# Performance work log

Measured on AMD Instinct MI355X. Metric: run time of the kernel, lower is better.

The kernel has to match this reference:

```python
import jax, jax.numpy as jnp
import numpy as np

B, NPG = 128, 128          # graphs, nodes per graph
N = B * NPG                # total nodes
K = 16                     # kNN neighbors within cutoff
D = 256                    # embedding_depth
H, DH = 4, 32              # heads = num_layers, head dim = (D//2)//H
L = 4                      # num graph convolutions
NR = 50                    # num_radial
CUTOFF = 2.0
OUT = 3 + 100              # 3 + max_ntypes


def setup_inputs() -> dict:
    rng = np.random.default_rng(0)
    pos = rng.standard_normal((N, 3)).astype(np.float32)
    nbrs = np.zeros((N, K), np.int32)
    mask = np.zeros((N, K), np.float32)
    for g in range(B):  # per-graph kNN with radial cutoff (setup only, numpy)
        p = pos[g * NPG:(g + 1) * NPG]
        d2 = ((p[:, None, :] - p[None, :, :]) ** 2).sum(-1)
        np.fill_diagonal(d2, np.inf)
        idx = np.argsort(d2, axis=1)[:, :K]
        dk = np.sqrt(np.take_along_axis(d2, idx, 1))
        nbrs[g * NPG:(g + 1) * NPG] = idx + g * NPG
        mask[g * NPG:(g + 1) * NPG] = (dk <= CUTOFF).astype(np.float32)
    batch_idx = np.repeat(np.arange(B, dtype=np.int32), NPG)

    key = jax.random.key(0)
    ks = jax.random.split(key, 12)
    s = 0.02
    return {
        'encoding': jax.random.normal(ks[0], (B, D), jnp.float32),
        'pos': jnp.asarray(pos),
        'batch_idx': jnp.asarray(batch_idx),
        'neighbors': jnp.asarray(nbrs),
        'nbr_mask': jnp.asarray(mask),
        'W_in': jax.random.normal(ks[1], (D + 3, D), jnp.float32) * s,
        'b_in': jnp.zeros((D,), jnp.float32),
        'Wq': jax.random.normal(ks[2], (L, D, H * DH), jnp.float32) * s,
        'Wk': jax.random.normal(ks[3], (L, D, H * DH), jnp.float32) * s,
        'Wv': jax.random.normal(ks[4], (L, D, H * DH), jnp.float32) * s,
        'We': jax.random.normal(ks[5], (L, NR, H * DH), jnp.float32) * s,
        'Wo': jax.random.normal(ks[6], (L, H * DH, D), jnp.float32) * s,
        'bo': jnp.zeros((L, D), jnp.float32),
        'Wfc': jax.random.normal(ks[7], (L, D, D), jnp.float32) * s,
        'bfc': jnp.zeros((L, D), jnp.float32),
        'ln_g': jnp.ones((L, D), jnp.float32),
        'ln_b': jnp.zeros((L, D), jnp.float32),
        'W_out': jax.random.normal(ks[8], (D, OUT), jnp.float32) * s,
        'b_out': jnp.zeros((OUT,), jnp.float32),
    }


def reference(encoding, pos, batch_idx, neighbors, nbr_mask,
              W_in, b_in, Wq, Wk, Wv, We, Wo, bo, Wfc, bfc,
              ln_g, ln_b, W_out, b_out):
    # x = encoding.repeat_interleave(graph_sizes); x[:, 0] = 1
    x = encoding[batch_idx]                      # [N, D]
    x = x.at[:, 0].set(1.0)
    h = jnp.concatenate([x, pos], axis=-1) @ W_in + b_in   # concat pos, embed

    # gaussian radial basis of neighbor distances
    dvec = pos[neighbors] - pos[:, None, :]      # [N, K, 3]
    d = jnp.sqrt((dvec ** 2).sum(-1) + 1e-12)    # [N, K]
    centers = jnp.linspace(0.0, CUTOFF, NR)
    width = centers[1] - centers[0]
    rbf = jnp.exp(-0.5 * ((d[..., None] - centers) / width) ** 2)  # [N, K, NR]

    scale = 1.0 / jnp.sqrt(jnp.float32(DH))
    m = nbr_mask[..., None]                      # [N, K, 1]
    for l in range(L):                           # TransformerConv layers
        q = (h @ Wq[l]).reshape(N, H, DH)
        k = (h @ Wk[l]).reshape(N, H, DH)
        v = (h @ Wv[l]).reshape(N, H, DH)
        e = (rbf @ We[l]).reshape(N, K, H, DH)   # edge embedding
        kj = k[neighbors] + e                    # [N, K, H, DH]
        vj = v[neighbors] + e
        logits = jnp.einsum('nhd,nkhd->nkh', q, kj) * scale
        logits = jnp.where(m > 0, logits, -1e9)
        a = jax.nn.softmax(logits, axis=1) * m   # masked attention over K
        msg = jnp.einsum('nkh,nkhd->nhd', a, vj).reshape(N, H * DH)
        h = h + msg @ Wo[l] + bo[l]              # residual update
        mu = h.mean(-1, keepdims=True)
        var = h.var(-1, keepdims=True)
        h = ln_g[l] * (h - mu) / jnp.sqrt(var + 1e-5) + ln_b[l]
        h = jax.nn.gelu(h @ Wfc[l] + bfc[l])     # nodewise fc (1 layer)

    return h @ W_out + b_out                     # [N, 3 + max_ntypes]
```

## Files before the change

### kernel.cpp

```cpp
#include <hip/hip_runtime.h>
#include <hip/hip_bf16.h>
#include <math.h>

#define N_PTS 16384
#define NLAYER 4

typedef __attribute__((ext_vector_type(8))) short bfrag;
typedef __attribute__((ext_vector_type(4))) float f32x4;
typedef unsigned short ushort_t;
typedef unsigned int uint_t;

__device__ __forceinline__ ushort_t f2b(float f) {
  __hip_bfloat16 h = __float2bfloat16(f);
  return *reinterpret_cast<const ushort_t*>(&h);
}
__device__ __forceinline__ float b2f(ushort_t u) {
  union { uint_t i; float f; } c; c.i = ((uint_t)u) << 16; return c.f;
}
__device__ __forceinline__ float blo(uint_t u) {
  union { uint_t i; float f; } c; c.i = u << 16; return c.f;
}
__device__ __forceinline__ float bhi(uint_t u) {
  union { uint_t i; float f; } c; c.i = u & 0xffff0000u; return c.f;
}

__global__ __launch_bounds__(256) void base_kernel(
    const float* __restrict__ enc, const float* __restrict__ W_in,
    const float* __restrict__ b_in, float* __restrict__ base)
{
  int b = blockIdx.x, j = threadIdx.x;
  __shared__ float se[256];
  se[j] = enc[b * 256 + j];
  __syncthreads();
  float acc = b_in[j] + W_in[j];
  for (int i = 1; i < 256; ++i) acc += se[i] * W_in[i * 256 + j];
  base[b * 256 + j] = acc;
}

__global__ __launch_bounds__(256) void embed_kernel(
    const float* __restrict__ base, const int* __restrict__ batch_idx,
    const float* __restrict__ pos, const float* __restrict__ W_in,
    ushort_t* __restrict__ h_bf)
{
  int n = blockIdx.x, j = threadIdx.x;
  int b = batch_idx[n];
  float px = pos[n * 3 + 0], py = pos[n * 3 + 1], pz = pos[n * 3 + 2];
  float v = base[b * 256 + j]
      + px * W_in[256 * 256 + j] + py * W_in[257 * 256 + j] + pz * W_in[258 * 256 + j];
  h_bf[(size_t)n * 256 + j] = f2b(v);
}

__global__ __launch_bounds__(256) void prep_qkv(
    const float* __restrict__ Wq, const float* __restrict__ Wk,
    const float* __restrict__ Wv, const float* __restrict__ We,
    ushort_t* __restrict__ out)
{
  int idx = blockIdx.x * 256 + threadIdx.x;
  int l = idx / (640 * 256);
  int rem = idx - l * (640 * 256);
  int j = rem >> 8, k = rem & 255;
  float v = 0.f;
  if (j < 128) v = Wq[((size_t)l * 256 + k) * 128 + j];
  else if (j < 328) {
    int p = j - 128, hq = p / 50, r = p - hq * 50;
    const float* wq = &Wq[((size_t)l * 256 + k) * 128 + hq * 32];
    const float* we = &We[((size_t)l * 50 + r) * 128 + hq * 32];
#pragma unroll
    for (int d = 0; d < 32; ++d) v += wq[d] * we[d];
  } else if (j < 456) v = Wk[((size_t)l * 256 + k) * 128 + (j - 328)];
  else if (j < 584) v = Wv[((size_t)l * 256 + k) * 128 + (j - 456)];
  out[idx] = f2b(v);
}

__global__ __launch_bounds__(256) void prep_bcat(
    const float* __restrict__ We, const float* __restrict__ Wo, ushort_t* __restrict__ out)
{
  int idx = blockIdx.x * 256 + threadIdx.x;
  int l = idx / (256 * 384);
  int rem = idx - l * (256 * 384);
  int j = rem / 384, k2 = rem - j * 384;
  float v = 0.f;
  if (k2 < 128) v = Wo[((size_t)l * 128 + k2) * 256 + j];
  else if (k2 < 328) {
    int p = k2 - 128, hq = p / 50, r = p - hq * 50;
    const float* we = &We[((size_t)l * 50 + r) * 128 + hq * 32];
    const float* wo = &Wo[((size_t)l * 128 + hq * 32) * 256 + j];
#pragma unroll
    for (int d = 0; d < 32; ++d) v += we[d] * wo[(size_t)d * 256];
  }
  out[idx] = f2b(v);
}

__global__ __launch_bounds__(256) void prep_wfc(
    const float* __restrict__ Wfc, ushort_t* __restrict__ out)
{
  int idx = blockIdx.x * 256 + threadIdx.x;
  int l = idx >> 16, rem = idx & 65535;
  int j = rem >> 8, k = rem & 255;
  out[idx] = f2b(Wfc[((size_t)l * 256 + k) * 256 + j]);
}

__global__ __launch_bounds__(256) void prep_wout(
    const float* __restrict__ W_out, ushort_t* __restrict__ out)
{
  int idx = blockIdx.x * 256 + threadIdx.x;
  int j = idx >> 8, k = idx & 255;
  out[idx] = (j < 103) ? f2b(W_out[(size_t)k * 103 + j]) : (ushort_t)0;
}

template<int MODE>
__global__ __launch_bounds__(512, 4) void fused_layer(
    const ushort_t* __restrict__ A0,
    const ushort_t* __restrict__ BcT,
    const float* __restrict__ bo,
    ushort_t* __restrict__ hb,
    const float* __restrict__ lg, const float* __restrict__ lb,
    const ushort_t* __restrict__ WfT,
    const float* __restrict__ bfc,
    const ushort_t* __restrict__ W3T,
    const float* __restrict__ b3,
    ushort_t* __restrict__ qext_b, ushort_t* __restrict__ kvb,
    float* __restrict__ outF)
{
  __shared__ __align__(16) ushort_t sA[32 * 384];
  __shared__ __align__(16) ushort_t sH[32 * 256];
  __shared__ float pS[8][32], pSS[8][32];

  const int tid = threadIdx.x;
  const int bid = blockIdx.x;
  const int lane = tid & 63, w = tid >> 6;
  const int l15 = lane & 15, l4 = lane >> 4;
  const int m0 = ((bid & 7) + 8 * ((bid >> 3) & 15)) * 128 + (bid >> 7) * 32;
  const int r7 = l15 & 7;

  f32x4 acc[2][2];

  if constexpr (MODE != 2) {
    for (int i = tid; i < 32 * 48; i += 512) {
      int r = i / 48, c8 = i - r * 48;
      uint4 v = (uint4){0, 0, 0, 0};
      if (c8 < 44) v = *(const uint4*)(A0 + (size_t)(m0 + r) * 352 + c8 * 8);
      *(uint4*)(&sA[r * 384 + ((c8 ^ (r & 7)) << 3)]) = v;
    }
    __syncthreads();

#pragma unroll
    for (int m = 0; m < 2; ++m) {
      acc[m][0] = (f32x4){0.f, 0.f, 0.f, 0.f};
      acc[m][1] = (f32x4){0.f, 0.f, 0.f, 0.f};
    }
    {
      const ushort_t* bB0 = BcT + (size_t)(w * 32 + l15) * 384 + l4 * 8;
      const ushort_t* bB1 = bB0 + 16 * 384;
#pragma unroll
      for (int k0 = 0; k0 < 352; k0 += 32) {
        const int ch = (k0 >> 3) + l4;
        bfrag a0 = *(const bfrag*)(sA + (0 * 16 + l15) * 384 + ((ch ^ r7) << 3));
        bfrag a1 = *(const bfrag*)(sA + (1 * 16 + l15) * 384 + ((ch ^ r7) << 3));
        bfrag b0 = *(const bfrag*)(bB0 + k0);
        bfrag b1 = *(const bfrag*)(bB1 + k0);
        acc[0][0] = __builtin_amdgcn_mfma_f32_16x16x32_bf16(a0, b0, acc[0][0], 0, 0, 0);
        acc[0][1] = __builtin_amdgcn_mfma_f32_16x16x32_bf16(a0, b1, acc[0][1], 0, 0, 0);
        acc[1][0] = __builtin_amdgcn_mfma_f32_16x16x32_bf16(a1, b0, acc[1][0], 0, 0, 0);
        acc[1][1] = __builtin_amdgcn_mfma_f32_16x16x32_bf16(a1, b1, acc[1][1], 0, 0, 0);
      }
    }

    const int c0 = w * 32 + l15, c1 = c0 + 16;
    {
      const float bo0 = bo[c0], bo1 = bo[c1];
#pragma unroll
      for (int m = 0; m < 2; ++m)
#pragma unroll
        for (int i = 0; i < 4; ++i) {
          const int rl = m * 16 + l4 * 4 + i;
          const size_t r = (size_t)(m0 + rl);
          float x0 = acc[m][0][i] + bo0 + b2f(hb[r * 256 + c0]);
          float x1 = acc[m][1][i] + bo1 + b2f(hb[r * 256 + c1]);
          acc[m][0][i] = x0; acc[m][1][i] = x1;
          float s = x0 + x1, ss = x0 * x0 + x1 * x1;
          s += __shfl_xor(s, 1, 64); ss += __shfl_xor(ss, 1, 64);
          s += __shfl_xor(s, 2, 64); ss += __shfl_xor(ss, 2, 64);
          s += __shfl_xor(s, 4, 64); ss += __shfl_xor(ss, 4, 64);
          s += __shfl_xor(s, 8, 64); ss += __shfl_xor(ss, 8, 64);
          if (l15 == 0) { pS[w][rl] = s; pSS[w][rl] = ss; }
        }
    }
    __syncthreads();
    {
      const float g0 = lg[c0], g1 = lg[c1];
      const float b0 = lb[c0], b1 = lb[c1];
      const int ch0 = c0 >> 3, ch1 = c1 >> 3;
#pragma unroll
      for (int m = 0; m < 2; ++m)
#pragma unroll
        for (int i = 0; i < 4; ++i) {
          const int rl = m * 16 + l4 * 4 + i;
          float s = 0.f, ss = 0.f;
#pragma unroll
          for (int w2 = 0; w2 < 8; ++w2) { s += pS[w2][rl]; ss += pSS[w2][rl]; }
          float mu = s * (1.f / 256.f);
          float var = ss * (1.f / 256.f) - mu * mu;
          float inv = 1.0f / sqrtf(var + 1e-5f);
          sH[rl * 256 + (((ch0 ^ (rl & 7)) << 3) | (c0 & 7))] =
              f2b(g0 * (acc[m][0][i] - mu) * inv + b0);
          sH[rl * 256 + (((ch1 ^ (rl & 7)) << 3) | (c1 & 7))] =
              f2b(g1 * (acc[m][1][i] - mu) * inv + b1);
        }
    }
    __syncthreads();

#pragma unroll
    for (int m = 0; m < 2; ++m) {
      acc[m][0] = (f32x4){0.f, 0.f, 0.f, 0.f};
      acc[m][1] = (f32x4){0.f, 0.f, 0.f, 0.f};
    }
    {
      const ushort_t* bB0 = WfT + (size_t)(w * 32 + l15) * 256 + l4 * 8;
      const ushort_t* bB1 = bB0 + 16 * 256;
#pragma unroll
      for (int k0 = 0; k0 < 256; k0 += 32) {
        const int ch = (k0 >> 3) + l4;
        bfrag a0 = *(const bfrag*)(sH + (0 * 16 + l15) * 256 + ((ch ^ r7) << 3));
        bfrag a1 = *(const bfrag*)(sH + (1 * 16 + l15) * 256 + ((ch ^ r7) << 3));
        bfrag b0 = *(const bfrag*)(bB0 + k0);
        bfrag b1 = *(const bfrag*)(bB1 + k0);
        acc[0][0] = __builtin_amdgcn_mfma_f32_16x16x32_bf16(a0, b0, acc[0][0], 0, 0, 0);
        acc[0][1] = __builtin_amdgcn_mfma_f32_16x16x32_bf16(a0, b1, acc[0][1], 0, 0, 0);
        acc[1][0] = __builtin_amdgcn_mfma_f32_16x16x32_bf16(a1, b0, acc[1][0], 0, 0, 0);
        acc[1][1] = __builtin_amdgcn_mfma_f32_16x16x32_bf16(a1, b1, acc[1][1], 0, 0, 0);
      }
    }

    {
      const float bf0 = bfc[c0], bf1 = bfc[c1];
      const int ch0 = c0 >> 3, ch1 = c1 >> 3;
#pragma unroll
      for (int m = 0; m < 2; ++m)
#pragma unroll
        for (int i = 0; i < 4; ++i) {
          const int rl = m * 16 + l4 * 4 + i;
          const size_t r = (size_t)(m0 + rl);
          float x0 = acc[m][0][i] + bf0;
          float x1 = acc[m][1][i] + bf1;
          float t0 = tanhf(0.7978845608028654f * (x0 + 0.044715f * x0 * x0 * x0));
          float t1 = tanhf(0.7978845608028654f * (x1 + 0.044715f * x1 * x1 * x1));
          float gl0 = 0.5f * x0 * (1.f + t0);
          float gl1 = 0.5f * x1 * (1.f + t1);
          ushort_t u0 = f2b(gl0), u1 = f2b(gl1);
          hb[r * 256 + c0] = u0;
          hb[r * 256 + c1] = u1;
          sA[rl * 256 + (((ch0 ^ (rl & 7)) << 3) | (c0 & 7))] = u0;
          sA[rl * 256 + (((ch1 ^ (rl & 7)) << 3) | (c1 & 7))] = u1;
        }
    }
    __syncthreads();
  } else {
    for (int i = tid; i < 32 * 32; i += 512) {
      int r = i >> 5, c8 = i & 31;
      *(uint4*)(&sA[r * 256 + ((c8 ^ (r & 7)) << 3)]) =
          *(const uint4*)(A0 + (size_t)(m0 + r) * 256 + c8 * 8);
    }
    __syncthreads();
  }

  const int NB = (MODE == 1) ? 1 : 5;
  for (int nb = 0; nb < NB; ++nb) {
    f32x4 a3[2];
    a3[0] = (f32x4){0.f, 0.f, 0.f, 0.f};
    a3[1] = (f32x4){0.f, 0.f, 0.f, 0.f};
    const ushort_t* bB = W3T + (size_t)(nb * 128 + w * 16 + l15) * 256 + l4 * 8;
#pragma unroll
    for (int k0 = 0; k0 < 256; k0 += 32) {
      const int ch = (k0 >> 3) + l4;
      bfrag a0 = *(const bfrag*)(sA + (0 * 16 + l15) * 256 + ((ch ^ r7) << 3));
      bfrag a1 = *(const bfrag*)(sA + (1 * 16 + l15) * 256 + ((ch ^ r7) << 3));
      bfrag b0 = *(const bfrag*)(bB + k0);
      a3[0] = __builtin_amdgcn_mfma_f32_16x16x32_bf16(a0, b0, a3[0], 0, 0, 0);
      a3[1] = __builtin_amdgcn_mfma_f32_16x16x32_bf16(a1, b0, a3[1], 0, 0, 0);
    }
    const int c = nb * 128 + w * 16 + l15;
#pragma unroll
    for (int m = 0; m < 2; ++m)
#pragma unroll
      for (int i = 0; i < 4; ++i) {
        const size_t r = (size_t)(m0 + m * 16 + l4 * 4 + i);
        float v = a3[m][i];
        if constexpr (MODE == 1) {
          if (c < 103) outF[r * 103 + c] = v + b3[c];
        } else {
          if (c < 328) qext_b[r * 352 + c] = f2b(v);
          else if (c < 584) kvb[r * 256 + (c - 328)] = f2b(v);
        }
      }
  }
}

__global__ __launch_bounds__(256) void attn_kernel(
    const ushort_t* __restrict__ qext, const ushort_t* __restrict__ kvb,
    const float* __restrict__ pos, const int* __restrict__ nbrs,
    const float* __restrict__ mask, ushort_t* __restrict__ Amsg)
{
  __shared__ __align__(16) ushort_t sQ[4][128];
  __shared__ __align__(16) float    sQE[4][4][52];
  __shared__ __align__(16) ushort_t sRbf[4][16][52];
  __shared__ float sA[4][64];
  __shared__ float sD[4][16];
  __shared__ float sMk[4][16];
  __shared__ int   sNb[4][16];

  const int tid = threadIdx.x;
  const int bid = blockIdx.x;
  const int lane = tid & 63, w = tid >> 6;
  const int g = (bid & 7) + 8 * ((bid >> 3) & 15);
  const int q4 = bid >> 7;
  const int kk = lane >> 2, hh = lane & 3;

  for (int it = 0; it < 4; ++it) {
    const int n = g * 128 + q4 * 16 + w * 4 + it;
    if (lane < 16) {
      int nb = nbrs[n * 16 + lane];
      sNb[w][lane] = nb;
      sMk[w][lane] = mask[n * 16 + lane];
      float dx = pos[nb * 3 + 0] - pos[n * 3 + 0];
      float dy = pos[nb * 3 + 1] - pos[n * 3 + 1];
      float dz = pos[nb * 3 + 2] - pos[n * 3 + 2];
      sD[w][lane] = sqrtf(dx * dx + dy * dy + dz * dz + 1e-12f);
      sRbf[w][lane][50] = 0; sRbf[w][lane][51] = 0;
      *(uint4*)(&sQ[w][lane * 8]) = *(const uint4*)(qext + (size_t)n * 352 + lane * 8);
    }
    if (lane < 50) {
      uint2 u = *(const uint2*)(qext + (size_t)n * 352 + 128 + lane * 4);
      int p = lane * 4;
#pragma unroll
      for (int e = 0; e < 4; ++e) {
        ushort_t bb = ((const ushort_t*)&u)[e];
        int pp = p + e, h2 = pp / 50, r = pp - h2 * 50;
        sQE[w][h2][r] = b2f(bb);
      }
    }
    if (lane < 8) sQE[w][lane >> 1][50 + (lane & 1)] = 0.f;
    {
      int kk2 = lane & 15;
      float dk = sD[w][kk2];
      int r0 = lane >> 4;
#pragma unroll
      for (int j = 0; j < 13; ++j) {
        int r = r0 + j * 4;
        if (r < 50) {
          float t = (dk - (2.f / 49.f) * (float)r) * 24.5f;
          sRbf[w][kk2][r] = f2b(__expf(-0.5f * t * t));
        }
      }
    }
    const int nb = sNb[w][kk];
    const ushort_t* krow = kvb + (size_t)nb * 256 + hh * 32;
    float qk = 0.f;
#pragma unroll
    for (int c8 = 0; c8 < 4; ++c8) {
      uint4 kv4 = *(const uint4*)(krow + c8 * 8);
      const uint_t* q4p = (const uint_t*)(&sQ[w][hh * 32 + c8 * 8]);
      uint_t qa = q4p[0], qb = q4p[1], qc = q4p[2], qd = q4p[3];
      qk += blo(qa) * blo(kv4.x) + bhi(qa) * bhi(kv4.x)
          + blo(qb) * blo(kv4.y) + bhi(qb) * bhi(kv4.y)
          + blo(qc) * blo(kv4.z) + bhi(qc) * bhi(kv4.z)
          + blo(qd) * blo(kv4.w) + bhi(qd) * bhi(kv4.w);
    }
    float qe = 0.f;
#pragma unroll
    for (int c = 0; c < 13; ++c) {
      float4 qv = *(const float4*)(&sQE[w][hh][c * 4]);
      uint2 rv = *(const uint2*)(&sRbf[w][kk][c * 4]);
      qe += qv.x * blo(rv.x) + qv.y * bhi(rv.x)
          + qv.z * blo(rv.y) + qv.w * bhi(rv.y);
    }
    float lg = 0.17677669529663687f * (qk + qe);
    lg = (sMk[w][kk] > 0.f) ? lg : -1e9f;

    float mx = lg;
#pragma unroll
    for (int off = 4; off < 64; off <<= 1) mx = fmaxf(mx, __shfl_xor(mx, off, 64));
    float ex = __expf(lg - mx);
    float sm = ex;
#pragma unroll
    for (int off = 4; off < 64; off <<= 1) sm += __shfl_xor(sm, off, 64);
    sA[w][kk * 4 + hh] = ex / sm * sMk[w][kk];

    if (lane < 50) {
      float r0 = 0.f, r1 = 0.f, r2 = 0.f, r3 = 0.f;
#pragma unroll
      for (int k2 = 0; k2 < 16; ++k2) {
        float rb = b2f(sRbf[w][k2][lane]);
        r0 += sA[w][k2 * 4 + 0] * rb;
        r1 += sA[w][k2 * 4 + 1] * rb;
        r2 += sA[w][k2 * 4 + 2] * rb;
        r3 += sA[w][k2 * 4 + 3] * rb;
      }
      Amsg[(size_t)n * 352 + 128 + 0 * 50 + lane] = f2b(r0);
      Amsg[(size_t)n * 352 + 128 + 1 * 50 + lane] = f2b(r1);
      Amsg[(size_t)n * 352 + 128 + 2 * 50 + lane] = f2b(r2);
      Amsg[(size_t)n * 352 + 128 + 3 * 50 + lane] = f2b(r3);
    }
    {
      const int h2 = lane >> 4;
      float m0v = 0.f, m1v = 0.f;
#pragma unroll
      for (int k2 = 0; k2 < 16; ++k2) {
        int nb2 = sNb[w][k2];
        uint_t vv = *(const uint_t*)(kvb + (size_t)nb2 * 256 + 128 + lane * 2);
        float a = sA[w][k2 * 4 + h2];
        m0v += a * blo(vv);
        m1v += a * bhi(vv);
      }
      uint_t o = (uint_t)f2b(m0v) | ((uint_t)f2b(m1v) << 16);
      *(uint_t*)(&Amsg[(size_t)n * 352 + lane * 2]) = o;
    }
    if (lane < 24) Amsg[(size_t)n * 352 + 328 + lane] = 0;
  }
}

extern "C" void kernel_launch(void* const* d_in, const int* in_sizes, int n_in,
                              void* d_out, int out_size, void* d_ws, size_t ws_size,
                              hipStream_t stream) {
  const float* enc    = (const float*)d_in[0];
  const float* pos    = (const float*)d_in[1];
  const int*   bidx   = (const int*)  d_in[2];
  const int*   nbrs   = (const int*)  d_in[3];
  const float* mask   = (const float*)d_in[4];
  const float* W_in   = (const float*)d_in[5];
  const float* b_in   = (const float*)d_in[6];
  const float* Wq     = (const float*)d_in[7];
  const float* Wk     = (const float*)d_in[8];
  const float* Wv     = (const float*)d_in[9];
  const float* We     = (const float*)d_in[10];
  const float* Wo     = (const float*)d_in[11];
  const float* bo     = (const float*)d_in[12];
  const float* Wfc    = (const float*)d_in[13];
  const float* bfc    = (const float*)d_in[14];
  const float* ln_g   = (const float*)d_in[15];
  const float* ln_b   = (const float*)d_in[16];
  const float* W_out  = (const float*)d_in[17];
  const float* b_out  = (const float*)d_in[18];
  float* out = (float*)d_out;

  const int N = N_PTS;
  ushort_t* ws = (ushort_t*)d_ws;
  ushort_t* hb     = ws;
  ushort_t* qext_b = hb + (size_t)N * 256;
  ushort_t* kvb    = qext_b + (size_t)N * 352;
  ushort_t* Amsg   = kvb + (size_t)N * 256;
  float*    base   = (float*)(Amsg + (size_t)N * 352);
  ushort_t* WqkvT  = (ushort_t*)(base + 128 * 256);
  ushort_t* BcT    = WqkvT + 4 * 640 * 256;
  ushort_t* WfT    = BcT  + 4 * 256 * 384;
  ushort_t* WoT    = WfT  + 4 * 256 * 256;

  base_kernel<<<128, 256, 0, stream>>>(enc, W_in, b_in, base);
  embed_kernel<<<N, 256, 0, stream>>>(base, bidx, pos, W_in, hb);
  prep_qkv<<<(4 * 640 * 256) / 256, 256, 0, stream>>>(Wq, Wk, Wv, We, WqkvT);
  prep_bcat<<<(4 * 256 * 384) / 256, 256, 0, stream>>>(We, Wo, BcT);
  prep_wfc<<<(4 * 256 * 256) / 256, 256, 0, stream>>>(Wfc, WfT);
  prep_wout<<<(128 * 256) / 256, 256, 0, stream>>>(W_out, WoT);

  fused_layer<2><<<N / 32, 512, 0, stream>>>(
      hb, nullptr, nullptr, nullptr, nullptr, nullptr, nullptr, nullptr,
      WqkvT, nullptr, qext_b, kvb, nullptr);

  for (int l = 0; l < NLAYER; ++l) {
    const ushort_t* BcT_l = BcT + (size_t)l * 256 * 384;
    const ushort_t* WfT_l = WfT + (size_t)l * 256 * 256;
    const float* bo_l  = bo  + (size_t)l * 256;
    const float* bfc_l = bfc + (size_t)l * 256;
    const float* lg_l  = ln_g + (size_t)l * 256;
    const float* lb_l  = ln_b + (size_t)l * 256;

    attn_kernel<<<1024, 256, 0, stream>>>(qext_b, kvb, pos, nbrs, mask, Amsg);

    if (l < NLAYER - 1) {
      const ushort_t* Wqkv_next = WqkvT + (size_t)(l + 1) * 640 * 256;
      fused_layer<0><<<N / 32, 512, 0, stream>>>(
          Amsg, BcT_l, bo_l, hb, lg_l, lb_l, WfT_l, bfc_l,
          Wqkv_next, nullptr, qext_b, kvb, nullptr);
    } else {
      fused_layer<1><<<N / 32, 512, 0, stream>>>(
          Amsg, BcT_l, bo_l, hb, lg_l, lb_l, WfT_l, bfc_l,
          WoT, b_out, nullptr, nullptr, out);
    }
  }
}
```

Before: 328.3 us.

## Stage weight tiles through LDS with async global_load_lds double buffering

The three GEMM phases of the fused layer kernel now copy their weight operand (BcT, WfT, W3T) into a double-buffered shared-memory tile with global_load_lds, prefetching the next k-slice while MFMAs run on the current one. Previously each wave read B fragments straight from global memory. Each k-step adds a block-wide barrier and an s_setprio bump around the MFMAs. The extra 32 KB of LDS and the per-step barriers may cut occupancy, which the launch bounds of 4 blocks per CU ask for.

```diff
diff --git a/kernel.cpp b/kernel.cpp
--- a/kernel.cpp
+++ b/kernel.cpp
@@ -23,6 +23,14 @@
 __device__ __forceinline__ float bhi(uint_t u) {
   union { uint_t i; float f; } c; c.i = u & 0xffff0000u; return c.f;
 }
+
+__device__ __forceinline__ void gload16(const ushort_t* g, ushort_t* l) {
+  __builtin_amdgcn_global_load_lds(
+      (const __attribute__((address_space(1))) unsigned int*)g,
+      (__attribute__((address_space(3))) unsigned int*)l, 16, 0, 0);
+}
+
+#define MFMA16(a, b, c) __builtin_amdgcn_mfma_f32_16x16x32_bf16((a), (b), (c), 0, 0, 0)
 
 __global__ __launch_bounds__(256) void base_kernel(
     const float* __restrict__ enc, const float* __restrict__ W_in,
@@ -124,6 +132,7 @@
 {
   __shared__ __align__(16) ushort_t sA[32 * 384];
   __shared__ __align__(16) ushort_t sH[32 * 256];
+  __shared__ __align__(16) ushort_t sB[2][8192];
   __shared__ float pS[8][32], pSS[8][32];
 
   const int tid = threadIdx.x;
@@ -132,10 +141,16 @@
   const int l15 = lane & 15, l4 = lane >> 4;
   const int m0 = ((bid & 7) + 8 * ((bid >> 3) & 15)) * 128 + (bid >> 7) * 32;
   const int r7 = l15 & 7;
+  const int q0 = w * 64 + lane;
 
   f32x4 acc[2][2];
 
   if constexpr (MODE != 2) {
+    gload16(BcT + (size_t)(q0 >> 2) * 384 + ((q0 & 3) << 3),
+            (ushort_t*)&sB[0][(w * 64) << 3]);
+    gload16(BcT + (size_t)((q0 + 512) >> 2) * 384 + (((q0 + 512) & 3) << 3),
+            (ushort_t*)&sB[0][(512 + w * 64) << 3]);
+
     for (int i = tid; i < 32 * 48; i += 512) {
       int r = i / 48, c8 = i - r * 48;
       uint4 v = (uint4){0, 0, 0, 0};
@@ -144,29 +159,42 @@
     }
     __syncthreads();
 
+    const int c0 = w * 32 + l15, c1 = c0 + 16;
+
 #pragma unroll
     for (int m = 0; m < 2; ++m) {
       acc[m][0] = (f32x4){0.f, 0.f, 0.f, 0.f};
       acc[m][1] = (f32x4){0.f, 0.f, 0.f, 0.f};
     }
-    {
-      const ushort_t* bB0 = BcT + (size_t)(w * 32 + l15) * 384 + l4 * 8;
-      const ushort_t* bB1 = bB0 + 16 * 384;
-#pragma unroll
-      for (int k0 = 0; k0 < 352; k0 += 32) {
-        const int ch = (k0 >> 3) + l4;
-        bfrag a0 = *(const bfrag*)(sA + (0 * 16 + l15) * 384 + ((ch ^ r7) << 3));
-        bfrag a1 = *(const bfrag*)(sA + (1 * 16 + l15) * 384 + ((ch ^ r7) << 3));
-        bfrag b0 = *(const bfrag*)(bB0 + k0);
-        bfrag b1 = *(const bfrag*)(bB1 + k0);
-        acc[0][0] = __builtin_amdgcn_mfma_f32_16x16x32_bf16(a0, b0, acc[0][0], 0, 0, 0);
-        acc[0][1] = __builtin_amdgcn_mfma_f32_16x16x32_bf16(a0, b1, acc[0][1], 0, 0, 0);
-        acc[1][0] = __builtin_amdgcn_mfma_f32_16x16x32_bf16(a1, b0, acc[1][0], 0, 0, 0);
-        acc[1][1] = __builtin_amdgcn_mfma_f32_16x16x32_bf16(a1, b1, acc[1][1], 0, 0, 0);
-      }
-    }
-
-    const int c0 = w * 32 + l15, c1 = c0 + 16;
+    for (int ks = 0; ks < 11; ++ks) {
+      if (ks < 10) {
+        const int k0n = (ks + 1) * 32;
+        ushort_t* db = (ushort_t*)sB[(ks + 1) & 1];
+        gload16(BcT + (size_t)(q0 >> 2) * 384 + k0n + ((q0 & 3) << 3),
+                db + ((w * 64) << 3));
+        gload16(BcT + (size_t)((q0 + 512) >> 2) * 384 + k0n + (((q0 + 512) & 3) << 3),
+                db + ((512 + w * 64) << 3));
+      }
+      const ushort_t* bbuf = sB[ks & 1];
+      const int ch = ((ks * 32) >> 3) + l4;
+      bfrag a0 = *(const bfrag*)(sA + l15 * 384 + ((ch ^ r7) << 3));
+      bfrag a1 = *(const bfrag*)(sA + (16 + l15) * 384 + ((ch ^ r7) << 3));
+      bfrag b0 = *(const bfrag*)(bbuf + ((c0 * 4 + l4) << 3));
+      bfrag b1 = *(const bfrag*)(bbuf + ((c1 * 4 + l4) << 3));
+      __builtin_amdgcn_s_setprio(1);
+      acc[0][0] = MFMA16(a0, b0, acc[0][0]);
+      acc[0][1] = MFMA16(a0, b1, acc[0][1]);
+      acc[1][0] = MFMA16(a1, b0, acc[1][0]);
+      acc[1][1] = MFMA16(a1, b1, acc[1][1]);
+      __builtin_amdgcn_s_setprio(0);
+      __syncthreads();
+    }
+
+    gload16(WfT + (size_t)(q0 >> 2) * 256 + ((q0 & 3) << 3),
+            (ushort_t*)&sB[0][(w * 64) << 3]);
+    gload16(WfT + (size_t)((q0 + 512) >> 2) * 256 + (((q0 + 512) & 3) << 3),
+            (ushort_t*)&sB[0][(512 + w * 64) << 3]);
+
     {
       const float bo0 = bo[c0], bo1 = bo[c1];
 #pragma unroll
@@ -215,22 +243,34 @@
       acc[m][0] = (f32x4){0.f, 0.f, 0.f, 0.f};
       acc[m][1] = (f32x4){0.f, 0.f, 0.f, 0.f};
     }
-    {
-      const ushort_t* bB0 = WfT + (size_t)(w * 32 + l15) * 256 + l4 * 8;
-      const ushort_t* bB1 = bB0 + 16 * 256;
-#pragma unroll
-      for (int k0 = 0; k0 < 256; k0 += 32) {
-        const int ch = (k0 >> 3) + l4;
-        bfrag a0 = *(const bfrag*)(sH + (0 * 16 + l15) * 256 + ((ch ^ r7) << 3));
-        bfrag a1 = *(const bfrag*)(sH + (1 * 16 + l15) * 256 + ((ch ^ r7) << 3));
-        bfrag b0 = *(const bfrag*)(bB0 + k0);
-        bfrag b1 = *(const bfrag*)(bB1 + k0);
-        acc[0][0] = __builtin_amdgcn_mfma_f32_16x16x32_bf16(a0, b0, acc[0][0], 0, 0, 0);
-        acc[0][1] = __builtin_amdgcn_mfma_f32_16x16x32_bf16(a0, b1, acc[0][1], 0, 0, 0);
-        acc[1][0] = __builtin_amdgcn_mfma_f32_16x16x32_bf16(a1, b0, acc[1][0], 0, 0, 0);
-        acc[1][1] = __builtin_amdgcn_mfma_f32_16x16x32_bf16(a1, b1, acc[1][1], 0, 0, 0);
-      }
-    }
+    for (int ks = 0; ks < 8; ++ks) {
+      if (ks < 7) {
+        const int k0n = (ks + 1) * 32;
+        ushort_t* db = (ushort_t*)sB[(ks + 1) & 1];
+        gload16(WfT + (size_t)(q0 >> 2) * 256 + k0n + ((q0 & 3) << 3),
+                db + ((w * 64) << 3));
+        gload16(WfT + (size_t)((q0 + 512) >> 2) * 256 + k0n + (((q0 + 512) & 3) << 3),
+                db + ((512 + w * 64) << 3));
+      }
+      const ushort_t* bbuf = sB[ks & 1];
+      const int ch = ((ks * 32) >> 3) + l4;
+      bfrag a0 = *(const bfrag*)(sH + l15 * 256 + ((ch ^ r7) << 3));
+      bfrag a1 = *(const bfrag*)(sH + (16 + l15) * 256 + ((ch ^ r7) << 3));
+      bfrag b0 = *(const bfrag*)(bbuf + ((c0 * 4 + l4) << 3));
+      bfrag b1 = *(const bfrag*)(bbuf + ((c1 * 4 + l4) << 3));
+      __builtin_amdgcn_s_setprio(1);
+      acc[0][0] = MFMA16(a0, b0, acc[0][0]);
+      acc[0][1] = MFMA16(a0, b1, acc[0][1]);
+      acc[1][0] = MFMA16(a1, b0, acc[1][0]);
+      acc[1][1] = MFMA16(a1, b1, acc[1][1]);
+      __builtin_amdgcn_s_setprio(0);
+      __syncthreads();
+    }
+
+    gload16(W3T + (size_t)(q0 & 127) * 256 + ((q0 >> 7) << 3),
+            (ushort_t*)&sB[0][(w * 64) << 3]);
+    gload16(W3T + (size_t)((q0 + 512) & 127) * 256 + (((q0 + 512) >> 7) << 3),
+            (ushort_t*)&sB[0][(512 + w * 64) << 3]);
 
     {
       const float bf0 = bfc[c0], bf1 = bfc[c1];
@@ -256,6 +296,10 @@
     }
     __syncthreads();
   } else {
+    gload16(W3T + (size_t)(q0 & 127) * 256 + ((q0 >> 7) << 3),
+            (ushort_t*)&sB[0][(w * 64) << 3]);
+    gload16(W3T + (size_t)((q0 + 512) & 127) * 256 + (((q0 + 512) >> 7) << 3),
+            (ushort_t*)&sB[0][(512 + w * 64) << 3]);
     for (int i = tid; i < 32 * 32; i += 512) {
       int r = i >> 5, c8 = i & 31;
       *(uint4*)(&sA[r * 256 + ((c8 ^ (r & 7)) << 3)]) =
@@ -264,35 +308,55 @@
     __syncthreads();
   }
 
-  const int NB = (MODE == 1) ? 1 : 5;
-  for (int nb = 0; nb < NB; ++nb) {
+  {
+    const int NPH = (MODE == 1) ? 4 : 20;
+    const int cl = w * 16 + l15;
     f32x4 a3[2];
     a3[0] = (f32x4){0.f, 0.f, 0.f, 0.f};
     a3[1] = (f32x4){0.f, 0.f, 0.f, 0.f};
-    const ushort_t* bB = W3T + (size_t)(nb * 128 + w * 16 + l15) * 256 + l4 * 8;
-#pragma unroll
-    for (int k0 = 0; k0 < 256; k0 += 32) {
-      const int ch = (k0 >> 3) + l4;
-      bfrag a0 = *(const bfrag*)(sA + (0 * 16 + l15) * 256 + ((ch ^ r7) << 3));
-      bfrag a1 = *(const bfrag*)(sA + (1 * 16 + l15) * 256 + ((ch ^ r7) << 3));
-      bfrag b0 = *(const bfrag*)(bB + k0);
-      a3[0] = __builtin_amdgcn_mfma_f32_16x16x32_bf16(a0, b0, a3[0], 0, 0, 0);
-      a3[1] = __builtin_amdgcn_mfma_f32_16x16x32_bf16(a1, b0, a3[1], 0, 0, 0);
-    }
-    const int c = nb * 128 + w * 16 + l15;
-#pragma unroll
-    for (int m = 0; m < 2; ++m)
-#pragma unroll
-      for (int i = 0; i < 4; ++i) {
-        const size_t r = (size_t)(m0 + m * 16 + l4 * 4 + i);
-        float v = a3[m][i];
-        if constexpr (MODE == 1) {
-          if (c < 103) outF[r * 103 + c] = v + b3[c];
-        } else {
-          if (c < 328) qext_b[r * 352 + c] = f2b(v);
-          else if (c < 584) kvb[r * 256 + (c - 328)] = f2b(v);
-        }
-      }
+    for (int p = 0; p < NPH; ++p) {
+      if (p + 1 < NPH) {
+        const int nb2 = (p + 1) >> 2, kp2 = (p + 1) & 3;
+        ushort_t* db = (ushort_t*)sB[(p + 1) & 1];
+        gload16(W3T + (size_t)(nb2 * 128 + (q0 & 127)) * 256 + kp2 * 64 + ((q0 >> 7) << 3),
+                db + ((w * 64) << 3));
+        gload16(W3T + (size_t)(nb2 * 128 + ((q0 + 512) & 127)) * 256 + kp2 * 64
+                    + (((q0 + 512) >> 7) << 3),
+                db + ((512 + w * 64) << 3));
+      }
+      const ushort_t* bbuf = sB[p & 1];
+      const int kp = p & 3;
+#pragma unroll
+      for (int t = 0; t < 2; ++t) {
+        const int kg = kp * 64 + t * 32;
+        const int ch = (kg >> 3) + l4;
+        bfrag a0 = *(const bfrag*)(sA + l15 * 256 + ((ch ^ r7) << 3));
+        bfrag a1 = *(const bfrag*)(sA + (16 + l15) * 256 + ((ch ^ r7) << 3));
+        bfrag b0 = *(const bfrag*)(bbuf + (((t * 4 + l4) * 128 + cl) << 3));
+        __builtin_amdgcn_s_setprio(1);
+        a3[0] = MFMA16(a0, b0, a3[0]);
+        a3[1] = MFMA16(a1, b0, a3[1]);
+        __builtin_amdgcn_s_setprio(0);
+      }
+      if (kp == 3) {
+        const int c = (p >> 2) * 128 + cl;
+#pragma unroll
+        for (int m = 0; m < 2; ++m)
+#pragma unroll
+          for (int i = 0; i < 4; ++i) {
+            const size_t r = (size_t)(m0 + m * 16 + l4 * 4 + i);
+            float v = a3[m][i];
+            if constexpr (MODE == 1) {
+              if (c < 103) outF[r * 103 + c] = v + b3[c];
+            } else {
+              if (c < 328) qext_b[r * 352 + c] = f2b(v);
+              else if (c < 584) kvb[r * 256 + (c - 328)] = f2b(v);
+            }
+            a3[m][i] = 0.f;
+          }
+      }
+      __syncthreads();
+    }
   }
 }
 
```

Result: no change. 325.2 us (median of 2 runs) (-0.9%).

## Prepack weights into MFMA fragment order and shrink fused layer to 16-row tiles

Applied to the files above, without the earlier changes.

Weights and the residual hidden state are stored pre-swizzled in MFMA B/accumulator fragment order, so each lane loads its fragment with one contiguous vector read and the LDS staging of A and B is gone. The fused layer now uses 128-thread blocks over 16 rows, keeps A fragments in registers with 8 column tiles per wave, and reduces LayerNorm statistics across only 2 waves. This trades larger per-thread register use and more global weight reads per row (less reuse across rows) for fewer LDS round-trips and barriers, plus higher block count.

```diff
diff --git a/kernel.cpp b/kernel.cpp
--- a/kernel.cpp
+++ b/kernel.cpp
@@ -23,6 +23,8 @@
 __device__ __forceinline__ float bhi(uint_t u) {
   union { uint_t i; float f; } c; c.i = u & 0xffff0000u; return c.f;
 }
+
+#define MFMA16(a, b, c) __builtin_amdgcn_mfma_f32_16x16x32_bf16((a), (b), (c), 0, 0, 0)
 
 __global__ __launch_bounds__(256) void base_kernel(
     const float* __restrict__ enc, const float* __restrict__ W_in,
@@ -40,14 +42,18 @@
 __global__ __launch_bounds__(256) void embed_kernel(
     const float* __restrict__ base, const int* __restrict__ batch_idx,
     const float* __restrict__ pos, const float* __restrict__ W_in,
-    ushort_t* __restrict__ h_bf)
+    ushort_t* __restrict__ h_bf, ushort_t* __restrict__ hbP)
 {
   int n = blockIdx.x, j = threadIdx.x;
   int b = batch_idx[n];
   float px = pos[n * 3 + 0], py = pos[n * 3 + 1], pz = pos[n * 3 + 2];
   float v = base[b * 256 + j]
       + px * W_in[256 * 256 + j] + py * W_in[257 * 256 + j] + pz * W_in[258 * 256 + j];
-  h_bf[(size_t)n * 256 + j] = f2b(v);
+  ushort_t u = f2b(v);
+  h_bf[(size_t)n * 256 + j] = u;
+  int rt = n >> 4, ct = j >> 4;
+  int lane = ((n & 15) >> 2) * 16 + (j & 15);
+  hbP[(((size_t)rt * 16 + ct) * 64 + lane) * 4 + (n & 3)] = u;
 }
 
 __global__ __launch_bounds__(256) void prep_qkv(
@@ -58,37 +64,42 @@
   int idx = blockIdx.x * 256 + threadIdx.x;
   int l = idx / (640 * 256);
   int rem = idx - l * (640 * 256);
-  int j = rem >> 8, k = rem & 255;
+  int c = rem >> 8, k = rem & 255;
   float v = 0.f;
-  if (j < 128) v = Wq[((size_t)l * 256 + k) * 128 + j];
-  else if (j < 328) {
-    int p = j - 128, hq = p / 50, r = p - hq * 50;
+  if (c < 128) v = Wq[((size_t)l * 256 + k) * 128 + c];
+  else if (c < 328) {
+    int p = c - 128, hq = p / 50, r = p - hq * 50;
     const float* wq = &Wq[((size_t)l * 256 + k) * 128 + hq * 32];
     const float* we = &We[((size_t)l * 50 + r) * 128 + hq * 32];
 #pragma unroll
     for (int d = 0; d < 32; ++d) v += wq[d] * we[d];
-  } else if (j < 456) v = Wk[((size_t)l * 256 + k) * 128 + (j - 328)];
-  else if (j < 584) v = Wv[((size_t)l * 256 + k) * 128 + (j - 456)];
-  out[idx] = f2b(v);
+  } else if (c < 456) v = Wk[((size_t)l * 256 + k) * 128 + (c - 328)];
+  else if (c < 584) v = Wv[((size_t)l * 256 + k) * 128 + (c - 456)];
+  size_t pos = (size_t)l * 163840
+      + (((c >> 4) * 8 + (k >> 5)) * 64 + ((k >> 3) & 3) * 16 + (c & 15)) * 8 + (k & 7);
+  out[pos] = f2b(v);
 }
 
 __global__ __launch_bounds__(256) void prep_bcat(
     const float* __restrict__ We, const float* __restrict__ Wo, ushort_t* __restrict__ out)
 {
   int idx = blockIdx.x * 256 + threadIdx.x;
-  int l = idx / (256 * 384);
-  int rem = idx - l * (256 * 384);
-  int j = rem / 384, k2 = rem - j * 384;
+  if (idx >= 4 * 256 * 352) return;
+  int l = idx / (256 * 352);
+  int rem = idx - l * (256 * 352);
+  int c = rem / 352, k = rem - c * 352;
   float v = 0.f;
-  if (k2 < 128) v = Wo[((size_t)l * 128 + k2) * 256 + j];
-  else if (k2 < 328) {
-    int p = k2 - 128, hq = p / 50, r = p - hq * 50;
+  if (k < 128) v = Wo[((size_t)l * 128 + k) * 256 + c];
+  else if (k < 328) {
+    int p = k - 128, hq = p / 50, r = p - hq * 50;
     const float* we = &We[((size_t)l * 50 + r) * 128 + hq * 32];
-    const float* wo = &Wo[((size_t)l * 128 + hq * 32) * 256 + j];
+    const float* wo = &Wo[((size_t)l * 128 + hq * 32) * 256 + c];
 #pragma unroll
     for (int d = 0; d < 32; ++d) v += we[d] * wo[(size_t)d * 256];
   }
-  out[idx] = f2b(v);
+  size_t pos = (size_t)l * 90112
+      + (((k >> 5) * 16 + (c >> 4)) * 64 + ((k >> 3) & 3) * 16 + (c & 15)) * 8 + (k & 7);
+  out[pos] = f2b(v);
 }
 
 __global__ __launch_bounds__(256) void prep_wfc(
@@ -96,196 +107,186 @@
 {
   int idx = blockIdx.x * 256 + threadIdx.x;
   int l = idx >> 16, rem = idx & 65535;
-  int j = rem >> 8, k = rem & 255;
-  out[idx] = f2b(Wfc[((size_t)l * 256 + k) * 256 + j]);
+  int c = rem >> 8, k = rem & 255;
+  float v = Wfc[((size_t)l * 256 + k) * 256 + c];
+  size_t pos = (size_t)l * 65536
+      + (((k >> 5) * 16 + (c >> 4)) * 64 + ((k >> 3) & 3) * 16 + (c & 15)) * 8 + (k & 7);
+  out[pos] = f2b(v);
 }
 
 __global__ __launch_bounds__(256) void prep_wout(
     const float* __restrict__ W_out, ushort_t* __restrict__ out)
 {
   int idx = blockIdx.x * 256 + threadIdx.x;
-  int j = idx >> 8, k = idx & 255;
-  out[idx] = (j < 103) ? f2b(W_out[(size_t)k * 103 + j]) : (ushort_t)0;
+  int c = idx >> 8, k = idx & 255;
+  float v = (c < 103) ? W_out[(size_t)k * 103 + c] : 0.f;
+  size_t pos = (((c >> 4) * 8 + (k >> 5)) * 64 + ((k >> 3) & 3) * 16 + (c & 15)) * 8 + (k & 7);
+  out[pos] = f2b(v);
 }
 
 template<int MODE>
-__global__ __launch_bounds__(512, 4) void fused_layer(
-    const ushort_t* __restrict__ A0,
-    const ushort_t* __restrict__ BcT,
+__global__ __launch_bounds__(128) void fused_layer(
+    const ushort_t* __restrict__ Amsg,
+    const ushort_t* __restrict__ BcP,
     const float* __restrict__ bo,
-    ushort_t* __restrict__ hb,
+    ushort_t* __restrict__ hbP,
     const float* __restrict__ lg, const float* __restrict__ lb,
-    const ushort_t* __restrict__ WfT,
+    const ushort_t* __restrict__ WfP,
     const float* __restrict__ bfc,
-    const ushort_t* __restrict__ W3T,
+    const ushort_t* __restrict__ W3P,
     const float* __restrict__ b3,
+    const ushort_t* __restrict__ h_bf,
     ushort_t* __restrict__ qext_b, ushort_t* __restrict__ kvb,
     float* __restrict__ outF)
 {
-  __shared__ __align__(16) ushort_t sA[32 * 384];
-  __shared__ __align__(16) ushort_t sH[32 * 256];
-  __shared__ float pS[8][32], pSS[8][32];
+  __shared__ __align__(16) ushort_t tb[16 * 264];
+  __shared__ float pS[2][16], pSS[2][16];
 
   const int tid = threadIdx.x;
-  const int bid = blockIdx.x;
-  const int lane = tid & 63, w = tid >> 6;
+  const int lane = tid & 63, wv = tid >> 6;
   const int l15 = lane & 15, l4 = lane >> 4;
-  const int m0 = ((bid & 7) + 8 * ((bid >> 3) & 15)) * 128 + (bid >> 7) * 32;
-  const int r7 = l15 & 7;
-
-  f32x4 acc[2][2];
+  const int rt = blockIdx.x;
+  const int r0 = rt * 16;
 
   if constexpr (MODE != 2) {
-    for (int i = tid; i < 32 * 48; i += 512) {
-      int r = i / 48, c8 = i - r * 48;
-      uint4 v = (uint4){0, 0, 0, 0};
-      if (c8 < 44) v = *(const uint4*)(A0 + (size_t)(m0 + r) * 352 + c8 * 8);
-      *(uint4*)(&sA[r * 384 + ((c8 ^ (r & 7)) << 3)]) = v;
+    const int cb = wv * 8;
+
+    bfrag aA[11];
+#pragma unroll
+    for (int ks = 0; ks < 11; ++ks)
+      aA[ks] = *(const bfrag*)(Amsg + (size_t)(r0 + l15) * 352 + ks * 32 + l4 * 8);
+
+    f32x4 acc[8];
+#pragma unroll
+    for (int j = 0; j < 8; ++j) acc[j] = (f32x4){0.f, 0.f, 0.f, 0.f};
+#pragma unroll
+    for (int ks = 0; ks < 11; ++ks) {
+#pragma unroll
+      for (int j = 0; j < 8; ++j) {
+        bfrag b = *(const bfrag*)(BcP + (((size_t)ks * 16 + cb + j) * 64 + lane) * 8);
+        acc[j] = MFMA16(aA[ks], b, acc[j]);
+      }
+    }
+
+    float s0 = 0.f, s1 = 0.f, s2 = 0.f, s3 = 0.f;
+    float q0 = 0.f, q1 = 0.f, q2 = 0.f, q3 = 0.f;
+#pragma unroll
+    for (int j = 0; j < 8; ++j) {
+      const int c = (cb + j) * 16 + l15;
+      const float boc = bo[c];
+      uint2 hv = *(const uint2*)(hbP + (((size_t)rt * 16 + cb + j) * 64 + lane) * 4);
+      const ushort_t* hu = (const ushort_t*)&hv;
+      float x0 = acc[j][0] + boc + b2f(hu[0]);
+      float x1 = acc[j][1] + boc + b2f(hu[1]);
+      float x2 = acc[j][2] + boc + b2f(hu[2]);
+      float x3 = acc[j][3] + boc + b2f(hu[3]);
+      acc[j][0] = x0; acc[j][1] = x1; acc[j][2] = x2; acc[j][3] = x3;
+      s0 += x0; q0 += x0 * x0; s1 += x1; q1 += x1 * x1;
+      s2 += x2; q2 += x2 * x2; s3 += x3; q3 += x3 * x3;
+    }
+#pragma unroll
+    for (int off = 1; off < 16; off <<= 1) {
+      s0 += __shfl_xor(s0, off, 64); q0 += __shfl_xor(q0, off, 64);
+      s1 += __shfl_xor(s1, off, 64); q1 += __shfl_xor(q1, off, 64);
+      s2 += __shfl_xor(s2, off, 64); q2 += __shfl_xor(q2, off, 64);
+      s3 += __shfl_xor(s3, off, 64); q3 += __shfl_xor(q3, off, 64);
+    }
+    if (l15 == 0) {
+      pS[wv][l4 * 4 + 0] = s0; pSS[wv][l4 * 4 + 0] = q0;
+      pS[wv][l4 * 4 + 1] = s1; pSS[wv][l4 * 4 + 1] = q1;
+      pS[wv][l4 * 4 + 2] = s2; pSS[wv][l4 * 4 + 2] = q2;
+      pS[wv][l4 * 4 + 3] = s3; pSS[wv][l4 * 4 + 3] = q3;
     }
     __syncthreads();
-
-#pragma unroll
-    for (int m = 0; m < 2; ++m) {
-      acc[m][0] = (f32x4){0.f, 0.f, 0.f, 0.f};
-      acc[m][1] = (f32x4){0.f, 0.f, 0.f, 0.f};
-    }
-    {
-      const ushort_t* bB0 = BcT + (size_t)(w * 32 + l15) * 384 + l4 * 8;
-      const ushort_t* bB1 = bB0 + 16 * 384;
-#pragma unroll
-      for (int k0 = 0; k0 < 352; k0 += 32) {
-        const int ch = (k0 >> 3) + l4;
-        bfrag a0 = *(const bfrag*)(sA + (0 * 16 + l15) * 384 + ((ch ^ r7) << 3));
-        bfrag a1 = *(const bfrag*)(sA + (1 * 16 + l15) * 384 + ((ch ^ r7) << 3));
-        bfrag b0 = *(const bfrag*)(bB0 + k0);
-        bfrag b1 = *(const bfrag*)(bB1 + k0);
-        acc[0][0] = __builtin_amdgcn_mfma_f32_16x16x32_bf16(a0, b0, acc[0][0], 0, 0, 0);
-        acc[0][1] = __builtin_amdgcn_mfma_f32_16x16x32_bf16(a0, b1, acc[0][1], 0, 0, 0);
-        acc[1][0] = __builtin_amdgcn_mfma_f32_16x16x32_bf16(a1, b0, acc[1][0], 0, 0, 0);
-        acc[1][1] = __builtin_amdgcn_mfma_f32_16x16x32_bf16(a1, b1, acc[1][1], 0, 0, 0);
-      }
-    }
-
-    const int c0 = w * 32 + l15, c1 = c0 + 16;
-    {
-      const float bo0 = bo[c0], bo1 = bo[c1];
-#pragma unroll
-      for (int m = 0; m < 2; ++m)
-#pragma unroll
-        for (int i = 0; i < 4; ++i) {
-          const int rl = m * 16 + l4 * 4 + i;
-          const size_t r = (size_t)(m0 + rl);
-          float x0 = acc[m][0][i] + bo0 + b2f(hb[r * 256 + c0]);
-          float x1 = acc[m][1][i] + bo1 + b2f(hb[r * 256 + c1]);
-          acc[m][0][i] = x0; acc[m][1][i] = x1;
-          float s = x0 + x1, ss = x0 * x0 + x1 * x1;
-          s += __shfl_xor(s, 1, 64); ss += __shfl_xor(ss, 1, 64);
-          s += __shfl_xor(s, 2, 64); ss += __shfl_xor(ss, 2, 64);
-          s += __shfl_xor(s, 4, 64); ss += __shfl_xor(ss, 4, 64);
-          s += __shfl_xor(s, 8, 64); ss += __shfl_xor(ss, 8, 64);
-          if (l15 == 0) { pS[w][rl] = s; pSS[w][rl] = ss; }
-        }
+    float mu[4], inv[4];
+#pragma unroll
+    for (int i = 0; i < 4; ++i) {
+      const int r = l4 * 4 + i;
+      float S = pS[0][r] + pS[1][r];
+      float Q = pSS[0][r] + pSS[1][r];
+      float m = S * (1.f / 256.f);
+      float var = Q * (1.f / 256.f) - m * m;
+      mu[i] = m;
+      inv[i] = 1.0f / sqrtf(var + 1e-5f);
+    }
+#pragma unroll
+    for (int j = 0; j < 8; ++j) {
+      const int c = (cb + j) * 16 + l15;
+      const float g = lg[c], bb = lb[c];
+#pragma unroll
+      for (int i = 0; i < 4; ++i)
+        tb[(l4 * 4 + i) * 264 + c] = f2b(g * (acc[j][i] - mu[i]) * inv[i] + bb);
     }
     __syncthreads();
-    {
-      const float g0 = lg[c0], g1 = lg[c1];
-      const float b0 = lb[c0], b1 = lb[c1];
-      const int ch0 = c0 >> 3, ch1 = c1 >> 3;
-#pragma unroll
-      for (int m = 0; m < 2; ++m)
-#pragma unroll
-        for (int i = 0; i < 4; ++i) {
-          const int rl = m * 16 + l4 * 4 + i;
-          float s = 0.f, ss = 0.f;
-#pragma unroll
-          for (int w2 = 0; w2 < 8; ++w2) { s += pS[w2][rl]; ss += pSS[w2][rl]; }
-          float mu = s * (1.f / 256.f);
-          float var = ss * (1.f / 256.f) - mu * mu;
-          float inv = 1.0f / sqrtf(var + 1e-5f);
-          sH[rl * 256 + (((ch0 ^ (rl & 7)) << 3) | (c0 & 7))] =
-              f2b(g0 * (acc[m][0][i] - mu) * inv + b0);
-          sH[rl * 256 + (((ch1 ^ (rl & 7)) << 3) | (c1 & 7))] =
-              f2b(g1 * (acc[m][1][i] - mu) * inv + b1);
-        }
-    }
+
+    bfrag aH[8];
+#pragma unroll
+    for (int ks = 0; ks < 8; ++ks)
+      aH[ks] = *(const bfrag*)(tb + l15 * 264 + ks * 32 + l4 * 8);
     __syncthreads();
 
 #pragma unroll
-    for (int m = 0; m < 2; ++m) {
-      acc[m][0] = (f32x4){0.f, 0.f, 0.f, 0.f};
-      acc[m][1] = (f32x4){0.f, 0.f, 0.f, 0.f};
-    }
-    {
-      const ushort_t* bB0 = WfT + (size_t)(w * 32 + l15) * 256 + l4 * 8;
-      const ushort_t* bB1 = bB0 + 16 * 256;
-#pragma unroll
-      for (int k0 = 0; k0 < 256; k0 += 32) {
-        const int ch = (k0 >> 3) + l4;
-        bfrag a0 = *(const bfrag*)(sH + (0 * 16 + l15) * 256 + ((ch ^ r7) << 3));
-        bfrag a1 = *(const bfrag*)(sH + (1 * 16 + l15) * 256 + ((ch ^ r7) << 3));
-        bfrag b0 = *(const bfrag*)(bB0 + k0);
-        bfrag b1 = *(const bfrag*)(bB1 + k0);
-        acc[0][0] = __builtin_amdgcn_mfma_f32_16x16x32_bf16(a0, b0, acc[0][0], 0, 0, 0);
-        acc[0][1] = __builtin_amdgcn_mfma_f32_16x16x32_bf16(a0, b1, acc[0][1], 0, 0, 0);
-        acc[1][0] = __builtin_amdgcn_mfma_f32_16x16x32_bf16(a1, b0, acc[1][0], 0, 0, 0);
-        acc[1][1] = __builtin_amdgcn_mfma_f32_16x16x32_bf16(a1, b1, acc[1][1], 0, 0, 0);
-      }
-    }
-
-    {
-      const float bf0 = bfc[c0], bf1 = bfc[c1];
-      const int ch0 = c0 >> 3, ch1 = c1 >> 3;
-#pragma unroll
-      for (int m = 0; m < 2; ++m)
-#pragma unroll
-        for (int i = 0; i < 4; ++i) {
-          const int rl = m * 16 + l4 * 4 + i;
-          const size_t r = (size_t)(m0 + rl);
-          float x0 = acc[m][0][i] + bf0;
-          float x1 = acc[m][1][i] + bf1;
-          float t0 = tanhf(0.7978845608028654f * (x0 + 0.044715f * x0 * x0 * x0));
-          float t1 = tanhf(0.7978845608028654f * (x1 + 0.044715f * x1 * x1 * x1));
-          float gl0 = 0.5f * x0 * (1.f + t0);
-          float gl1 = 0.5f * x1 * (1.f + t1);
-          ushort_t u0 = f2b(gl0), u1 = f2b(gl1);
-          hb[r * 256 + c0] = u0;
-          hb[r * 256 + c1] = u1;
-          sA[rl * 256 + (((ch0 ^ (rl & 7)) << 3) | (c0 & 7))] = u0;
-          sA[rl * 256 + (((ch1 ^ (rl & 7)) << 3) | (c1 & 7))] = u1;
-        }
+    for (int j = 0; j < 8; ++j) acc[j] = (f32x4){0.f, 0.f, 0.f, 0.f};
+#pragma unroll
+    for (int ks = 0; ks < 8; ++ks) {
+#pragma unroll
+      for (int j = 0; j < 8; ++j) {
+        bfrag b = *(const bfrag*)(WfP + (((size_t)ks * 16 + cb + j) * 64 + lane) * 8);
+        acc[j] = MFMA16(aH[ks], b, acc[j]);
+      }
+    }
+
+#pragma unroll
+    for (int j = 0; j < 8; ++j) {
+      const int c = (cb + j) * 16 + l15;
+      const float bfcc = bfc[c];
+      ushort_t uo[4];
+#pragma unroll
+      for (int i = 0; i < 4; ++i) {
+        float x = acc[j][i] + bfcc;
+        float t = tanhf(0.7978845608028654f * (x + 0.044715f * x * x * x));
+        float gl = 0.5f * x * (1.f + t);
+        uo[i] = f2b(gl);
+        tb[(l4 * 4 + i) * 264 + c] = uo[i];
+      }
+      *(uint2*)(hbP + (((size_t)rt * 16 + cb + j) * 64 + lane) * 4) = *(const uint2*)uo;
     }
     __syncthreads();
+  }
+
+  bfrag aG[8];
+  if constexpr (MODE == 2) {
+#pragma unroll
+    for (int ks = 0; ks < 8; ++ks)
+      aG[ks] = *(const bfrag*)(h_bf + (size_t)(r0 + l15) * 256 + ks * 32 + l4 * 8);
   } else {
-    for (int i = tid; i < 32 * 32; i += 512) {
-      int r = i >> 5, c8 = i & 31;
-      *(uint4*)(&sA[r * 256 + ((c8 ^ (r & 7)) << 3)]) =
-          *(const uint4*)(A0 + (size_t)(m0 + r) * 256 + c8 * 8);
-    }
-    __syncthreads();
-  }
-
-  const int NB = (MODE == 1) ? 1 : 5;
-  for (int nb = 0; nb < NB; ++nb) {
-    f32x4 a3[2];
-    a3[0] = (f32x4){0.f, 0.f, 0.f, 0.f};
-    a3[1] = (f32x4){0.f, 0.f, 0.f, 0.f};
-    const ushort_t* bB = W3T + (size_t)(nb * 128 + w * 16 + l15) * 256 + l4 * 8;
-#pragma unroll
-    for (int k0 = 0; k0 < 256; k0 += 32) {
-      const int ch = (k0 >> 3) + l4;
-      bfrag a0 = *(const bfrag*)(sA + (0 * 16 + l15) * 256 + ((ch ^ r7) << 3));
-      bfrag a1 = *(const bfrag*)(sA + (1 * 16 + l15) * 256 + ((ch ^ r7) << 3));
-      bfrag b0 = *(const bfrag*)(bB + k0);
-      a3[0] = __builtin_amdgcn_mfma_f32_16x16x32_bf16(a0, b0, a3[0], 0, 0, 0);
-      a3[1] = __builtin_amdgcn_mfma_f32_16x16x32_bf16(a1, b0, a3[1], 0, 0, 0);
-    }
-    const int c = nb * 128 + w * 16 + l15;
-#pragma unroll
-    for (int m = 0; m < 2; ++m)
+#pragma unroll
+    for (int ks = 0; ks < 8; ++ks)
+      aG[ks] = *(const bfrag*)(tb + l15 * 264 + ks * 32 + l4 * 8);
+  }
+
+  const int NCT = (MODE == 1) ? 4 : 20;
+  const int cg = wv * NCT;
+  for (int ch = 0; ch < NCT; ch += 4) {
+    f32x4 a3[4];
+#pragma unroll
+    for (int j = 0; j < 4; ++j) a3[j] = (f32x4){0.f, 0.f, 0.f, 0.f};
+#pragma unroll
+    for (int ks = 0; ks < 8; ++ks) {
+#pragma unroll
+      for (int j = 0; j < 4; ++j) {
+        const int ct = cg + ch + j;
+        bfrag b = *(const bfrag*)(W3P + (((size_t)ct * 8 + ks) * 64 + lane) * 8);
+        a3[j] = MFMA16(aG[ks], b, a3[j]);
+      }
+    }
+#pragma unroll
+    for (int j = 0; j < 4; ++j) {
+      const int c = (cg + ch + j) * 16 + l15;
 #pragma unroll
       for (int i = 0; i < 4; ++i) {
-        const size_t r = (size_t)(m0 + m * 16 + l4 * 4 + i);
-        float v = a3[m][i];
+        const size_t r = (size_t)(r0 + l4 * 4 + i);
+        float v = a3[j][i];
         if constexpr (MODE == 1) {
           if (c < 103) outF[r * 103 + c] = v + b3[c];
         } else {
@@ -293,6 +294,7 @@
           else if (c < 584) kvb[r * 256 + (c - 328)] = f2b(v);
         }
       }
+    }
   }
 }
 
@@ -445,30 +447,31 @@
 
   const int N = N_PTS;
   ushort_t* ws = (ushort_t*)d_ws;
-  ushort_t* hb     = ws;
-  ushort_t* qext_b = hb + (size_t)N * 256;
+  ushort_t* hbP    = ws;
+  ushort_t* h_bf   = hbP + (size_t)N * 256;
+  ushort_t* qext_b = h_bf + (size_t)N * 256;
   ushort_t* kvb    = qext_b + (size_t)N * 352;
   ushort_t* Amsg   = kvb + (size_t)N * 256;
   float*    base   = (float*)(Amsg + (size_t)N * 352);
-  ushort_t* WqkvT  = (ushort_t*)(base + 128 * 256);
-  ushort_t* BcT    = WqkvT + 4 * 640 * 256;
-  ushort_t* WfT    = BcT  + 4 * 256 * 384;
-  ushort_t* WoT    = WfT  + 4 * 256 * 256;
+  ushort_t* W3P    = (ushort_t*)(base + 128 * 256);
+  ushort_t* BcP    = W3P + 4 * 163840;
+  ushort_t* WfP    = BcP + 4 * 90112;
+  ushort_t* WoP    = WfP + 4 * 65536;
 
   base_kernel<<<128, 256, 0, stream>>>(enc, W_in, b_in, base);
-  embed_kernel<<<N, 256, 0, stream>>>(base, bidx, pos, W_in, hb);
-  prep_qkv<<<(4 * 640 * 256) / 256, 256, 0, stream>>>(Wq, Wk, Wv, We, WqkvT);
-  prep_bcat<<<(4 * 256 * 384) / 256, 256, 0, stream>>>(We, Wo, BcT);
-  prep_wfc<<<(4 * 256 * 256) / 256, 256, 0, stream>>>(Wfc, WfT);
-  prep_wout<<<(128 * 256) / 256, 256, 0, stream>>>(W_out, WoT);
-
-  fused_layer<2><<<N / 32, 512, 0, stream>>>(
-      hb, nullptr, nullptr, nullptr, nullptr, nullptr, nullptr, nullptr,
-      WqkvT, nullptr, qext_b, kvb, nullptr);
+  embed_kernel<<<N, 256, 0, stream>>>(base, bidx, pos, W_in, h_bf, hbP);
+  prep_qkv<<<(4 * 640 * 256) / 256, 256, 0, stream>>>(Wq, Wk, Wv, We, W3P);
+  prep_bcat<<<(4 * 256 * 352 + 255) / 256, 256, 0, stream>>>(We, Wo, BcP);
+  prep_wfc<<<(4 * 256 * 256) / 256, 256, 0, stream>>>(Wfc, WfP);
+  prep_wout<<<(128 * 256) / 256, 256, 0, stream>>>(W_out, WoP);
+
+  fused_layer<2><<<N / 16, 128, 0, stream>>>(
+      nullptr, nullptr, nullptr, nullptr, nullptr, nullptr, nullptr, nullptr,
+      W3P, nullptr, h_bf, qext_b, kvb, nullptr);
 
   for (int l = 0; l < NLAYER; ++l) {
-    const ushort_t* BcT_l = BcT + (size_t)l * 256 * 384;
-    const ushort_t* WfT_l = WfT + (size_t)l * 256 * 256;
+    const ushort_t* BcP_l = BcP + (size_t)l * 90112;
+    const ushort_t* WfP_l = WfP + (size_t)l * 65536;
     const float* bo_l  = bo  + (size_t)l * 256;
     const float* bfc_l = bfc + (size_t)l * 256;
     const float* lg_l  = ln_g + (size_t)l * 256;
@@ -477,14 +480,14 @@
     attn_kernel<<<1024, 256, 0, stream>>>(qext_b, kvb, pos, nbrs, mask, Amsg);
 
     if (l < NLAYER - 1) {
-      const ushort_t* Wqkv_next = WqkvT + (size_t)(l + 1) * 640 * 256;
-      fused_layer<0><<<N / 32, 512, 0, stream>>>(
-          Amsg, BcT_l, bo_l, hb, lg_l, lb_l, WfT_l, bfc_l,
-          Wqkv_next, nullptr, qext_b, kvb, nullptr);
+      const ushort_t* W3P_next = W3P + (size_t)(l + 1) * 163840;
+      fused_layer<0><<<N / 16, 128, 0, stream>>>(
+          Amsg, BcP_l, bo_l, hbP, lg_l, lb_l, WfP_l, bfc_l,
+          W3P_next, nullptr, nullptr, qext_b, kvb, nullptr);
     } else {
-      fused_layer<1><<<N / 32, 512, 0, stream>>>(
-          Amsg, BcT_l, bo_l, hb, lg_l, lb_l, WfT_l, bfc_l,
-          WoT, b_out, nullptr, nullptr, out);
-    }
-  }
-}
+      fused_layer<1><<<N / 16, 128, 0, stream>>>(
+          Amsg, BcP_l, bo_l, hbP, lg_l, lb_l, WfP_l, bfc_l,
+          WoP, b_out, nullptr, nullptr, nullptr, out);
+    }
+  }
+}
```

After: 370.7 us. 1.13x slower.
